# Optimization experiments

Measured on AMD Instinct MI355X. Metric: run time of the kernel, lower is better.

## Reference

```python
import jax, jax.numpy as jnp
import numpy as np

B, N = 4096, 8192
PULSE_LO = 40.0 / 60.0   # Hz
PULSE_HI = 250.0 / 60.0  # Hz


def setup_inputs() -> dict:
    key = jax.random.key(0)
    k1, k2 = jax.random.split(key)
    outputs = jax.random.normal(k1, (B, N), dtype=jnp.float32)
    # reference heart rates in Hz, uniform inside the pulse band
    targets = jax.random.uniform(k2, (B, 1), dtype=jnp.float32,
                                 minval=PULSE_LO, maxval=PULSE_HI)
    return {"outputs": outputs, "targets": targets, "Fs": 20}


def reference(outputs, targets, Fs):
    n = outputs.shape[-1]
    F = n // 2 + 1
    f = jnp.linspace(0.0, Fs / 2.0, F, dtype=jnp.float32)  # [F]

    min_idx = jnp.argmin(jnp.abs(f - PULSE_LO))
    max_idx = jnp.argmin(jnp.abs(f - PULSE_HI))

    # normalized rFFT power spectrum (torch.rfft(..., normalized=True) divides by sqrt(N))
    X = jnp.fft.rfft(outputs) * (1.0 / np.sqrt(n))          # [B, F] complex
    P1 = X.real ** 2 + X.imag ** 2                          # [B, F]

    # per-sample reference bin index
    r = jnp.argmin(jnp.abs(f[None, :] - targets.reshape(-1, 1)), axis=1)  # [B]
    rb = r[:, None]                                         # [B, 1]
    i = jnp.arange(F)[None, :]                              # [1, F]

    # signal mask u: 1 at ref and 1st harmonic, 0.5 at ref+-1 (applied after, as in torch)
    u = jnp.where((i == rb - 1) | (i == rb + 1), 0.5,
                  jnp.where((i == rb) | (i == 2 * rb), 1.0, 0.0))
    # noise mask w = 1 - u, zeroed outside pulse band and around 1st harmonic
    w = jnp.where((i < min_idx) | (i >= max_idx) |
                  (i == 2 * rb - 1) | (i == 2 * rb + 1),
                  0.0, 1.0 - u)

    signal_energy = jnp.sum(P1 * u, axis=1)                 # [B]
    noise_energy = jnp.sum(P1 * w, axis=1)                  # [B]
    losses = -10.0 * jnp.log(signal_energy / (noise_energy + 1.0)) / jnp.log(10.0)
    return jnp.mean(losses)
```

## Files before the change

### kernel.cpp

```cpp
#include <hip/hip_runtime.h>
#include <math.h>

#define TPB 256
#define NCX 4096

__device__ __forceinline__ float2 cmul(float2 a, float2 b) {
    return make_float2(a.x * b.x - a.y * b.y, a.x * b.y + a.y * b.x);
}

__device__ __forceinline__ int sw(int i) { return i ^ ((i >> 5) & 31); }

__device__ __forceinline__ void dft4(float2& a, float2& b, float2& c, float2& d) {
    float2 t0 = make_float2(a.x + c.x, a.y + c.y);
    float2 t1 = make_float2(a.x - c.x, a.y - c.y);
    float2 t2 = make_float2(b.x + d.x, b.y + d.y);
    float2 t3 = make_float2(b.x - d.x, b.y - d.y);
    a = make_float2(t0.x + t2.x, t0.y + t2.y);
    b = make_float2(t1.x + t3.y, t1.y - t3.x);
    c = make_float2(t0.x - t2.x, t0.y - t2.y);
    d = make_float2(t1.x - t3.y, t1.y + t3.x);
}

__device__ __forceinline__ void dft16(float2 v[16]) {
#pragma unroll
    for (int j = 0; j < 4; ++j) dft4(v[j], v[4 + j], v[8 + j], v[12 + j]);
    const float C1 = 0.9238795325112867f, S1 = 0.3826834323650898f;
    const float R2 = 0.7071067811865476f;
    v[5]  = cmul(v[5],  make_float2( C1, -S1));
    v[9]  = cmul(v[9],  make_float2( R2, -R2));
    v[13] = cmul(v[13], make_float2( S1, -C1));
    v[6]  = cmul(v[6],  make_float2( R2, -R2));
    v[10] = cmul(v[10], make_float2(0.f, -1.f));
    v[14] = cmul(v[14], make_float2(-R2, -R2));
    v[7]  = cmul(v[7],  make_float2( S1, -C1));
    v[11] = cmul(v[11], make_float2(-R2, -R2));
    v[15] = cmul(v[15], make_float2(-C1,  S1));
#pragma unroll
    for (int b = 0; b < 4; ++b) dft4(v[4 * b], v[4 * b + 1], v[4 * b + 2], v[4 * b + 3]);
}

__global__ __launch_bounds__(TPB, 4) void snr_kernel(const float* __restrict__ x,
                                                     const float* __restrict__ targets,
                                                     float* __restrict__ out) {
    __shared__ float re[NCX];
    __shared__ float im[NCX];
    __shared__ float spec[6];
    __shared__ float red[4];
    __shared__ int r_sh;

    const int t = threadIdx.x;
    const int blk = blockIdx.x;

    if (t == 0) {
        float tg = targets[blk];
        const float df = 0.00244140625f;
        int c0 = (int)(tg * 409.6f) - 2;
        if (c0 < 0) c0 = 0;
        int r = c0;
        float best = fabsf(df * (float)c0 - tg);
        for (int i = c0 + 1; i <= c0 + 4 && i <= 4096; ++i) {
            float dd = fabsf(df * (float)i - tg);
            if (dd < best) { best = dd; r = i; }
        }
        r_sh = r;
    }

    float2 v[16];
    const float2* row = (const float2*)(x + (size_t)blk * 8192);
#pragma unroll
    for (int l = 0; l < 16; ++l) v[l] = row[t + 256 * l];

    dft16(v);
    {
        float ang = -1.5339807878856412e-3f * (float)t;
        float sn, cs; __sincosf(ang, &sn, &cs);
        float2 w1 = make_float2(cs, sn);
        float2 w2 = cmul(w1, w1), w3 = cmul(w2, w1);
        float2 w4 = cmul(w2, w2), w8 = cmul(w4, w4), w12 = cmul(w8, w4);
        float2 wa[4] = {make_float2(1.f, 0.f), w1, w2, w3};
        float2 wb[4] = {make_float2(1.f, 0.f), w4, w8, w12};
#pragma unroll
        for (int m = 0; m < 16; ++m) {
            float2 y = cmul(v[4 * (m & 3) + (m >> 2)], cmul(wb[m >> 2], wa[m & 3]));
            int idx = sw(16 * t + m);
            re[idx] = y.x; im[idx] = y.y;
        }
    }
    __syncthreads();

#pragma unroll
    for (int l = 0; l < 16; ++l) { int idx = sw(t + 256 * l); v[l] = make_float2(re[idx], im[idx]); }
    __syncthreads();
    dft16(v);
    {
        const int p = t >> 4, q = t & 15;
        float ang = -0.02454369260617026f * (float)p;
        float sn, cs; __sincosf(ang, &sn, &cs);
        float2 w1 = make_float2(cs, sn);
        float2 w2 = cmul(w1, w1), w3 = cmul(w2, w1);
        float2 w4 = cmul(w2, w2), w8 = cmul(w4, w4), w12 = cmul(w8, w4);
        float2 wa[4] = {make_float2(1.f, 0.f), w1, w2, w3};
        float2 wb[4] = {make_float2(1.f, 0.f), w4, w8, w12};
#pragma unroll
        for (int m = 0; m < 16; ++m) {
            float2 y = cmul(v[4 * (m & 3) + (m >> 2)], cmul(wb[m >> 2], wa[m & 3]));
            int idx = sw(q + 256 * p + 16 * m);
            re[idx] = y.x; im[idx] = y.y;
        }
    }
    __syncthreads();

#pragma unroll
    for (int l = 0; l < 16; ++l) { int idx = sw(t + 256 * l); v[l] = make_float2(re[idx], im[idx]); }
    __syncthreads();
    dft16(v);
#pragma unroll
    for (int m = 0; m < 16; ++m) {
        float2 y = v[4 * (m & 3) + (m >> 2)];
        int idx = sw(t + 256 * m);
        re[idx] = y.x; im[idx] = y.y;
    }
    __syncthreads();

    const int r = r_sh;
    const int r2 = 2 * r;
    float band = 0.f;
    {
        float ang = -7.669903939428206e-4f * (float)t;
        float sn, cs; __sincosf(ang, &sn, &cs);
        float2 wk = make_float2(cs, sn);
        const float2 wstep = make_float2(0.9807852804032304f, -0.19509032201612825f);
#pragma unroll
        for (int m = 0; m < 16; ++m) {
            int k = t + 256 * m;
            int i1 = sw(k);
            int i2 = sw((4096 - k) & 4095);
            float2 Zk = make_float2(re[i1], im[i1]);
            float2 Zn = make_float2(re[i2], im[i2]);
            float sx = Zk.x + Zn.x, sy = Zk.y - Zn.y;
            float dx = Zk.x - Zn.x, dy = Zk.y + Zn.y;
            float tx = dx * wk.x - dy * wk.y;
            float ty = dx * wk.y + dy * wk.x;
            float Xr = 0.5f * (sx + ty);
            float Xi = 0.5f * (sy - tx);
            float P = (Xr * Xr + Xi * Xi) * (1.0f / 8192.0f);
            if ((unsigned)(k - 273) <= 1433u) band += P;
            int d1 = k - (r - 1);
            if ((unsigned)d1 < 3u) spec[d1] = P;
            int d2 = k - (r2 - 1);
            if ((unsigned)d2 < 3u) spec[3 + d2] = P;
            wk = cmul(wk, wstep);
        }
    }

#pragma unroll
    for (int off = 32; off > 0; off >>= 1) band += __shfl_down(band, off);
    if ((t & 63) == 0) red[t >> 6] = band;
    __syncthreads();

    if (t == 0) {
        float bb = red[0] + red[1] + red[2] + red[3];
        float S = spec[1] + spec[4] + 0.5f * (spec[0] + spec[2]);
        float noise = bb;
        if (r <= 1706)      noise -= spec[1];
        if (r - 1 >= 273)   noise -= 0.5f * spec[0];
        if (r + 1 <= 1706)  noise -= 0.5f * spec[2];
        if (r2 - 1 <= 1706) noise -= spec[3];
        if (r2 <= 1706)     noise -= spec[4];
        if (r2 + 1 <= 1706) noise -= spec[5];
        float loss = -10.0f * log10f(S / (noise + 1.0f));
        atomicAdd(out, loss * (1.0f / 4096.0f));
    }
}

extern "C" void kernel_launch(void* const* d_in, const int* in_sizes, int n_in,
                              void* d_out, int out_size, void* d_ws, size_t ws_size,
                              hipStream_t stream) {
    const float* x = (const float*)d_in[0];
    const float* tg = (const float*)d_in[1];
    float* out = (float*)d_out;
    hipMemsetAsync(out, 0, sizeof(float), stream);
    snr_kernel<<<4096, TPB, 0, stream>>>(x, tg, out);
}
```

Before: 214.4 us.

## Fuse final FFT pass with post-processing by computing mirrored columns in registers

Shared memory switches from split re/im arrays to an interleaved float2 buffer with a new swizzle, and the small spec/red/r_sh arrays are folded into that same buffer. The last radix-16 pass is run twice per thread, on its own column and on the mirrored column (256-t), so the real-FFT post-processing reads Z[k] and Z[N-k] from registers. This drops the final shared-memory write, one barrier and the mirrored shared reads. It doubles that pass's arithmetic and register use, while launch bounds are raised to 5 blocks per SM to try to increase occupancy.

```diff
diff --git a/kernel.cpp b/kernel.cpp
--- a/kernel.cpp
+++ b/kernel.cpp
@@ -2,13 +2,12 @@
 #include <math.h>
 
 #define TPB 256
-#define NCX 4096
 
 __device__ __forceinline__ float2 cmul(float2 a, float2 b) {
     return make_float2(a.x * b.x - a.y * b.y, a.x * b.y + a.y * b.x);
 }
 
-__device__ __forceinline__ int sw(int i) { return i ^ ((i >> 5) & 31); }
+__device__ __forceinline__ int sw2(int i) { return i ^ ((i >> 4) & 15); }
 
 __device__ __forceinline__ void dft4(float2& a, float2& b, float2& c, float2& d) {
     float2 t0 = make_float2(a.x + c.x, a.y + c.y);
@@ -39,30 +38,27 @@
     for (int b = 0; b < 4; ++b) dft4(v[4 * b], v[4 * b + 1], v[4 * b + 2], v[4 * b + 3]);
 }
 
-__global__ __launch_bounds__(TPB, 4) void snr_kernel(const float* __restrict__ x,
+__global__ __launch_bounds__(TPB, 5) void snr_kernel(const float* __restrict__ x,
                                                      const float* __restrict__ targets,
                                                      float* __restrict__ out) {
-    __shared__ float re[NCX];
-    __shared__ float im[NCX];
-    __shared__ float spec[6];
-    __shared__ float red[4];
-    __shared__ int r_sh;
+    __shared__ __align__(16) float2 Z[4096];
+    float* zf = (float*)Z;
 
     const int t = threadIdx.x;
     const int blk = blockIdx.x;
 
-    if (t == 0) {
+    int r;
+    {
         float tg = targets[blk];
         const float df = 0.00244140625f;
         int c0 = (int)(tg * 409.6f) - 2;
         if (c0 < 0) c0 = 0;
-        int r = c0;
+        r = c0;
         float best = fabsf(df * (float)c0 - tg);
         for (int i = c0 + 1; i <= c0 + 4 && i <= 4096; ++i) {
             float dd = fabsf(df * (float)i - tg);
             if (dd < best) { best = dd; r = i; }
         }
-        r_sh = r;
     }
 
     float2 v[16];
@@ -81,15 +77,13 @@
         float2 wb[4] = {make_float2(1.f, 0.f), w4, w8, w12};
 #pragma unroll
         for (int m = 0; m < 16; ++m) {
-            float2 y = cmul(v[4 * (m & 3) + (m >> 2)], cmul(wb[m >> 2], wa[m & 3]));
-            int idx = sw(16 * t + m);
-            re[idx] = y.x; im[idx] = y.y;
+            Z[sw2(16 * t + m)] = cmul(v[4 * (m & 3) + (m >> 2)], cmul(wb[m >> 2], wa[m & 3]));
         }
     }
     __syncthreads();
 
 #pragma unroll
-    for (int l = 0; l < 16; ++l) { int idx = sw(t + 256 * l); v[l] = make_float2(re[idx], im[idx]); }
+    for (int l = 0; l < 16; ++l) v[l] = Z[sw2(t + 256 * l)];
     __syncthreads();
     dft16(v);
     {
@@ -103,26 +97,21 @@
         float2 wb[4] = {make_float2(1.f, 0.f), w4, w8, w12};
 #pragma unroll
         for (int m = 0; m < 16; ++m) {
-            float2 y = cmul(v[4 * (m & 3) + (m >> 2)], cmul(wb[m >> 2], wa[m & 3]));
-            int idx = sw(q + 256 * p + 16 * m);
-            re[idx] = y.x; im[idx] = y.y;
+            Z[sw2(q + 256 * p + 16 * m)] = cmul(v[4 * (m & 3) + (m >> 2)], cmul(wb[m >> 2], wa[m & 3]));
         }
     }
     __syncthreads();
 
+    float2 va[16], vb[16];
+    const int tp = (256 - t) & 255;
 #pragma unroll
-    for (int l = 0; l < 16; ++l) { int idx = sw(t + 256 * l); v[l] = make_float2(re[idx], im[idx]); }
+    for (int l = 0; l < 16; ++l) va[l] = Z[sw2(t + 256 * l)];
+#pragma unroll
+    for (int l = 0; l < 16; ++l) vb[l] = Z[sw2(tp + 256 * l)];
     __syncthreads();
-    dft16(v);
-#pragma unroll
-    for (int m = 0; m < 16; ++m) {
-        float2 y = v[4 * (m & 3) + (m >> 2)];
-        int idx = sw(t + 256 * m);
-        re[idx] = y.x; im[idx] = y.y;
-    }
-    __syncthreads();
+    dft16(va);
+    dft16(vb);
 
-    const int r = r_sh;
     const int r2 = 2 * r;
     float band = 0.f;
     {
@@ -133,10 +122,9 @@
 #pragma unroll
         for (int m = 0; m < 16; ++m) {
             int k = t + 256 * m;
-            int i1 = sw(k);
-            int i2 = sw((4096 - k) & 4095);
-            float2 Zk = make_float2(re[i1], im[i1]);
-            float2 Zn = make_float2(re[i2], im[i2]);
+            float2 Zk = va[4 * (m & 3) + (m >> 2)];
+            int mp = (t == 0) ? ((16 - m) & 15) : (15 - m);
+            float2 Zn = vb[4 * (mp & 3) + (mp >> 2)];
             float sx = Zk.x + Zn.x, sy = Zk.y - Zn.y;
             float dx = Zk.x - Zn.x, dy = Zk.y + Zn.y;
             float tx = dx * wk.x - dy * wk.y;
@@ -146,28 +134,28 @@
             float P = (Xr * Xr + Xi * Xi) * (1.0f / 8192.0f);
             if ((unsigned)(k - 273) <= 1433u) band += P;
             int d1 = k - (r - 1);
-            if ((unsigned)d1 < 3u) spec[d1] = P;
+            if ((unsigned)d1 < 3u) zf[d1] = P;
             int d2 = k - (r2 - 1);
-            if ((unsigned)d2 < 3u) spec[3 + d2] = P;
+            if ((unsigned)d2 < 3u) zf[3 + d2] = P;
             wk = cmul(wk, wstep);
         }
     }
 
 #pragma unroll
     for (int off = 32; off > 0; off >>= 1) band += __shfl_down(band, off);
-    if ((t & 63) == 0) red[t >> 6] = band;
+    if ((t & 63) == 0) zf[8 + (t >> 6)] = band;
     __syncthreads();
 
     if (t == 0) {
-        float bb = red[0] + red[1] + red[2] + red[3];
-        float S = spec[1] + spec[4] + 0.5f * (spec[0] + spec[2]);
+        float bb = zf[8] + zf[9] + zf[10] + zf[11];
+        float S = zf[1] + zf[4] + 0.5f * (zf[0] + zf[2]);
         float noise = bb;
-        if (r <= 1706)      noise -= spec[1];
-        if (r - 1 >= 273)   noise -= 0.5f * spec[0];
-        if (r + 1 <= 1706)  noise -= 0.5f * spec[2];
-        if (r2 - 1 <= 1706) noise -= spec[3];
-        if (r2 <= 1706)     noise -= spec[4];
-        if (r2 + 1 <= 1706) noise -= spec[5];
+        if (r <= 1706)      noise -= zf[1];
+        if (r - 1 >= 273)   noise -= 0.5f * zf[0];
+        if (r + 1 <= 1706)  noise -= 0.5f * zf[2];
+        if (r2 - 1 <= 1706) noise -= zf[3];
+        if (r2 <= 1706)     noise -= zf[4];
+        if (r2 + 1 <= 1706) noise -= zf[5];
         float loss = -10.0f * log10f(S / (noise + 1.0f));
         atomicAdd(out, loss * (1.0f / 4096.0f));
     }
```

New measurement: 316.2 us. +47.5%, slower.
